# Kernel optimization log

Hardware: AMD Instinct MI355X
Metric: run time of the kernel (lower is better)

The kernel has to match this reference:

```python
import jax, jax.numpy as jnp
import numpy as np

BOUNDS = [0.01, 1.0, 100.0]
STEPS = [128, 128]
ALPHA_C = 0.01          # cfg.renderer.alpha
N_IMPORTANCE = 128      # cfg.renderer.importance_steps
N_RAYS = 65536


def _zvals_log_coarse():
    # matches torch.linspace(log10(b[i]), log10(b[i+1]) - seg/steps[i], steps[i]) per segment
    segs = []
    for i, s in enumerate(STEPS):
        lo = np.log10(BOUNDS[i]); hi = np.log10(BOUNDS[i + 1])
        segs.append(np.linspace(lo, hi - (hi - lo) / s, s, dtype=np.float32))
    return np.concatenate(segs)


def _seg_scale():
    tot = float(sum(STEPS))
    return np.concatenate([np.full(s, s / tot, dtype=np.float32) for s in STEPS])


def setup_inputs() -> dict:
    key = jax.random.key(0)
    k1, k2, k3, k4 = jax.random.split(key, 4)
    sigmas_coarse = jax.random.uniform(k1, (N_RAYS, sum(STEPS)), dtype=jnp.float32) * 5.0
    sigmas_fine = jax.random.uniform(k2, (N_RAYS, N_IMPORTANCE), dtype=jnp.float32) * 5.0
    rgbs_fine = jax.random.uniform(k3, (N_RAYS, N_IMPORTANCE, 3), dtype=jnp.float32)
    bg_color = jax.random.uniform(k4, (3,), dtype=jnp.float32)
    return {"sigmas_coarse": sigmas_coarse, "sigmas_fine": sigmas_fine,
            "rgbs_fine": rgbs_fine, "bg_color": bg_color}


def _weights_from_sigmas(sigmas, z_log):
    # delta[:, :-1] = diff(z_log), last delta = 0 (as in efficient_sampling)
    delta = jnp.concatenate([z_log[:, 1:] - z_log[:, :-1], jnp.zeros_like(z_log[:, :1])], -1)
    alpha = 1.0 - jnp.exp(-sigmas * delta)
    alpha_shift = jnp.concatenate([jnp.zeros_like(alpha[:, :1]), alpha[:, :-1]], -1)
    trans = jnp.cumprod(1.0 - alpha_shift, axis=-1)   # transmittance
    return alpha * trans


def _reweight(weights):
    # pad with zeros, 3-tap max blur, floor by alpha/S, per-segment rescale, normalize
    wpad = jnp.pad(weights, ((0, 0), (1, 1)))
    w = 0.5 * (jnp.maximum(wpad[:, :-2], wpad[:, 1:-1]) + jnp.maximum(wpad[:, 1:-1], wpad[:, 2:]))
    w = w + ALPHA_C / w.shape[-1]
    w = w * jnp.asarray(_seg_scale())
    return w / jnp.sum(w, axis=-1, keepdims=True)


def _sample_pdf(bins, weights, n_samples):
    # weights already normalized -> pdf; deterministic stratified u for reproducibility
    cdf = jnp.cumsum(weights, axis=-1)                     # [N, S]
    u = (jnp.arange(n_samples, dtype=bins.dtype) + 0.5) / n_samples
    u = jnp.broadcast_to(u, (bins.shape[0], n_samples))    # [N, n]
    inds = jax.vmap(lambda c, uu: jnp.searchsorted(c, uu, side='right'))(cdf, u)
    S = bins.shape[-1]
    below = jnp.clip(inds - 1, 0, S - 1)
    above = jnp.clip(inds, 0, S - 1)
    cdf_b = jnp.take_along_axis(cdf, below, -1)
    cdf_a = jnp.take_along_axis(cdf, above, -1)
    bin_b = jnp.take_along_axis(bins, below, -1)
    bin_a = jnp.take_along_axis(bins, above, -1)
    denom = jnp.where(cdf_a - cdf_b < 1e-5, 1.0, cdf_a - cdf_b)
    t = (u - cdf_b) / denom
    return bin_b + t * (bin_a - bin_b)


def reference(sigmas_coarse, sigmas_fine, rgbs_fine, bg_color):
    # --- efficient_sampling (no_grad path) ---
    z_log = jnp.broadcast_to(jnp.asarray(_zvals_log_coarse()), sigmas_coarse.shape)
    w_coarse = _weights_from_sigmas(sigmas_coarse, z_log)
    w_re = _reweight(w_coarse)
    z_log_fine = _sample_pdf(z_log, w_re, N_IMPORTANCE)     # [N, n_imp], sorted
    z_fine = jnp.power(10.0, z_log_fine)
    # --- render_rays_log-style compositing on fine samples ---
    w_fine = _weights_from_sigmas(sigmas_fine, z_log_fine)
    image = jnp.einsum('ns,nsc->nc', w_fine, rgbs_fine)
    image = image + (1.0 - jnp.sum(w_fine, -1)[..., None]) * bg_color
    invdepth = jnp.sum(w_fine / z_fine, axis=-1)
    lo = np.float32(np.log10(BOUNDS[0])); hi = np.float32(np.log10(BOUNDS[-1]))
    z_log_s = (z_log_fine - lo) / (hi - lo)
    return image, invdepth, w_fine, z_log_s
```

## Files before the change

### kernel.cpp

```cpp
#include <hip/hip_runtime.h>

#define SC 256
#define NF 128

template<int CTRL, int RM, int BM>
__device__ __forceinline__ float dpp_add(float x) {
    int s = __builtin_amdgcn_update_dpp(0, __float_as_int(x), CTRL, RM, BM, true);
    return x + __int_as_float(s);
}
template<int CTRL, int RM, int BM>
__device__ __forceinline__ int dpp_imax(int x) {
    int s = __builtin_amdgcn_update_dpp(0, x, CTRL, RM, BM, true);
    return (x > s) ? x : s;
}
template<int CTRL>
__device__ __forceinline__ float dpp_mov0(float x) {
    return __int_as_float(__builtin_amdgcn_update_dpp(0, __float_as_int(x), CTRL, 0xF, 0xF, true));
}
__device__ __forceinline__ float lane_f(float x, int l) {
    return __int_as_float(__builtin_amdgcn_readlane(__float_as_int(x), l));
}

__device__ __forceinline__ float wave_incl_scan(float x) {
    x = dpp_add<0x111, 0xF, 0xF>(x);
    x = dpp_add<0x112, 0xF, 0xF>(x);
    x = dpp_add<0x114, 0xF, 0xF>(x);
    x = dpp_add<0x118, 0xF, 0xF>(x);
    x = dpp_add<0x142, 0xA, 0xF>(x);
    x = dpp_add<0x143, 0xC, 0xF>(x);
    return x;
}

__device__ __forceinline__ int wave_incl_scan_imax(int x) {
    x = dpp_imax<0x111, 0xF, 0xF>(x);
    x = dpp_imax<0x112, 0xF, 0xF>(x);
    x = dpp_imax<0x114, 0xF, 0xF>(x);
    x = dpp_imax<0x118, 0xF, 0xF>(x);
    x = dpp_imax<0x142, 0xA, 0xF>(x);
    x = dpp_imax<0x143, 0xC, 0xF>(x);
    return x;
}

__device__ __forceinline__ float wave_sum_lane0(float x) {
    x = dpp_add<0xB1, 0xF, 0xF>(x);
    x = dpp_add<0x4E, 0xF, 0xF>(x);
    x = dpp_add<0x124, 0xF, 0xF>(x);
    x = dpp_add<0x128, 0xF, 0xF>(x);
    return x + lane_f(x, 16) + lane_f(x, 32) + lane_f(x, 48);
}

__device__ __forceinline__ int bin_klo(float c) {
    int k = (int)ceilf(fmaf(128.0f, c, -0.5f));
    return (k < 0) ? 0 : k;
}

__global__ __launch_bounds__(256) void nerf_render_kernel(
    const float* __restrict__ sig_c,
    const float* __restrict__ sig_f,
    const float* __restrict__ rgb_f,
    const float* __restrict__ bg,
    float* __restrict__ out,
    int n_rays)
{
    const int lane = threadIdx.x & 63;
    const int wid  = threadIdx.x >> 6;
    const int ray  = (blockIdx.x << 2) + wid;
    if (ray >= n_rays) return;

    __shared__ float s_cdf[4][SC];
    __shared__ int   s_idx[4][NF];

    const float4 sc4 = *reinterpret_cast<const float4*>(sig_c + (size_t)ray * SC + 4 * lane);
    const float2 sf  = *reinterpret_cast<const float2*>(sig_f + (size_t)ray * NF + 2 * lane);
    const float2* rp = reinterpret_cast<const float2*>(rgb_f + (size_t)ray * (NF * 3) + 6 * lane);
    const float2 ra = rp[0], rb = rp[1], rc = rp[2];
    const float bg0 = bg[0], bg1 = bg[1], bg2 = bg[2];

    const float DLT = 0.015625f;
    float x0 = sc4.x * DLT;
    float x1 = sc4.y * DLT;
    float x2 = sc4.z * DLT;
    float x3 = (lane == 63) ? 0.0f : sc4.w * DLT;

    float p0 = x0, p1 = p0 + x1, p2 = p1 + x2, p3 = p2 + x3;
    float incl = wave_incl_scan(p3);
    float excl = incl - p3;

    float T0 = __expf(-excl);
    float T1 = __expf(-(excl + p0));
    float T2 = __expf(-(excl + p1));
    float T3 = __expf(-(excl + p2));
    float T4 = __expf(-(excl + p3));
    float w0 = T0 - T1, w1 = T1 - T2, w2 = T2 - T3, w3 = T3 - T4;

    float wl = dpp_mov0<0x138>(w3);
    float wr = dpp_mov0<0x130>(w0);

    const float FLOOR = 0.01f / 256.0f;
    float m01 = fmaxf(w0, w1), m12 = fmaxf(w1, w2), m23 = fmaxf(w2, w3);
    float r0 = 0.5f * (fmaxf(wl, w0) + m01) + FLOOR;
    float r1 = 0.5f * (m01 + m12) + FLOOR;
    float r2 = 0.5f * (m12 + m23) + FLOOR;
    float r3 = 0.5f * (m23 + fmaxf(w3, wr)) + FLOOR;

    float q0 = r0, q1 = q0 + r1, q2 = q1 + r2, q3 = q2 + r3;
    float incl2 = wave_incl_scan(q3);
    float excl2 = incl2 - q3;
    float total = lane_f(incl2, 63);
    float inv_total = __builtin_amdgcn_rcpf(total);

    float c0 = (excl2 + q0) * inv_total;
    float c1 = (excl2 + q1) * inv_total;
    float c2 = (excl2 + q2) * inv_total;
    float c3 = (excl2 + q3) * inv_total;
    float cprev = dpp_mov0<0x138>(c3);

    float* cdf = s_cdf[wid];
    int*   idx = s_idx[wid];

    *reinterpret_cast<float4*>(&cdf[4 * lane]) = make_float4(c0, c1, c2, c3);

    *reinterpret_cast<int2*>(&idx[2 * lane]) = make_int2(-1, -1);

    const int jb = 4 * lane;
    int k0 = bin_klo(cprev);
    int k1 = bin_klo(c0);
    int k2 = bin_klo(c1);
    int k3 = bin_klo(c2);
    int k4 = bin_klo(c3);
    if (k0 < k1 && k0 < NF) idx[k0] = jb + 0;
    if (k1 < k2 && k1 < NF) idx[k1] = jb + 1;
    if (k2 < k3 && k2 < NF) idx[k2] = jb + 2;
    if (k3 < k4 && k3 < NF) idx[k3] = jb + 3;

    __asm__ __volatile__("" ::: "memory");

    const int2 jraw = *reinterpret_cast<const int2*>(&idx[2 * lane]);
    int m  = (jraw.x > jraw.y) ? jraw.x : jraw.y;
    int M  = wave_incl_scan_imax(m);
    int E  = __builtin_amdgcn_update_dpp(0, M, 0x138, 0xF, 0xF, true);
    int j0 = (E  > jraw.x) ? E  : jraw.x;
    int j1 = (j0 > jraw.y) ? j0 : jraw.y;

    int b0 = (j0 > 0) ? j0 - 1 : 0;
    int b1 = (j1 > 0) ? j1 - 1 : 0;
    float ca0 = cdf[j0], cb0 = cdf[b0];
    float ca1 = cdf[j1], cb1 = cdf[b1];

    const float u0 = ((float)(2 * lane) + 0.5f) * 0.0078125f;
    const float u1 = ((float)(2 * lane) + 1.5f) * 0.0078125f;

    float dn0 = ca0 - cb0;  dn0 = (dn0 < 1e-5f) ? 1.0f : dn0;
    float dn1 = ca1 - cb1;  dn1 = (dn1 < 1e-5f) ? 1.0f : dn1;
    float sc0f = (j0 > 0) ? DLT : 0.0f;
    float sc1f = (j1 > 0) ? DLT : 0.0f;
    float zL0 = fmaf((float)b0, DLT, -2.0f);
    float zL1 = fmaf((float)b1, DLT, -2.0f);
    float zl0 = fmaf((u0 - cb0) * __builtin_amdgcn_rcpf(dn0), sc0f, zL0);
    float zl1 = fmaf((u1 - cb1) * __builtin_amdgcn_rcpf(dn1), sc1f, zL1);

    float znext = dpp_mov0<0x130>(zl0);
    float d0 = zl1 - zl0;
    float d1 = (lane == 63) ? 0.0f : (znext - zl1);

    float y0 = sf.x * d0;
    float y1 = sf.y * d1;
    float ps = y0 + y1;
    float fincl = wave_incl_scan(ps);
    float fexcl = fincl - ps;

    float U0 = __expf(-fexcl);
    float U1 = __expf(-(fexcl + y0));
    float U2 = __expf(-(fexcl + ps));
    float wf0 = U0 - U1, wf1 = U1 - U2;

    float img_r = wf0 * ra.x + wf1 * rb.y;
    float img_g = wf0 * ra.y + wf1 * rc.x;
    float img_b = wf0 * rb.x + wf1 * rc.y;
    float wsum  = wf0 + wf1;
    float invd = wf0 * __exp10f(-zl0) + wf1 * __exp10f(-zl1);

    img_r = wave_sum_lane0(img_r);
    img_g = wave_sum_lane0(img_g);
    img_b = wave_sum_lane0(img_b);
    wsum  = wave_sum_lane0(wsum);
    invd  = wave_sum_lane0(invd);

    float* out_img  = out;
    float* out_invd = out + (size_t)n_rays * 3;
    float* out_wf   = out + (size_t)n_rays * 4;
    float* out_zs   = out + (size_t)n_rays * 4 + (size_t)n_rays * NF;

    if (lane == 0) {
        float one_m = 1.0f - wsum;
        out_img[(size_t)ray * 3 + 0] = img_r + one_m * bg0;
        out_img[(size_t)ray * 3 + 1] = img_g + one_m * bg1;
        out_img[(size_t)ray * 3 + 2] = img_b + one_m * bg2;
        out_invd[ray] = invd;
    }
    *reinterpret_cast<float2*>(out_wf + (size_t)ray * NF + 2 * lane) =
        make_float2(wf0, wf1);
    *reinterpret_cast<float2*>(out_zs + (size_t)ray * NF + 2 * lane) =
        make_float2((zl0 + 2.0f) * 0.25f, (zl1 + 2.0f) * 0.25f);
}

extern "C" void kernel_launch(void* const* d_in, const int* in_sizes, int n_in,
                              void* d_out, int out_size, void* d_ws, size_t ws_size,
                              hipStream_t stream) {
    const float* sig_c = (const float*)d_in[0];
    const float* sig_f = (const float*)d_in[1];
    const float* rgb_f = (const float*)d_in[2];
    const float* bg    = (const float*)d_in[3];
    float* out = (float*)d_out;

    const int n_rays = in_sizes[1] / NF;
    dim3 grid((n_rays + 3) / 4), block(256);
    hipLaunchKernelGGL(nerf_render_kernel, grid, block, 0, stream,
                       sig_c, sig_f, rgb_f, bg, out, n_rays);
}
```

Measured before the change: 236.3 us.

## Make kernel persistent with software-prefetched double-buffered ray loads

```diff
diff --git a/kernel.cpp b/kernel.cpp
--- a/kernel.cpp
+++ b/kernel.cpp
@@ -54,33 +54,35 @@
     return (k < 0) ? 0 : k;
 }
 
-__global__ __launch_bounds__(256) void nerf_render_kernel(
-    const float* __restrict__ sig_c,
-    const float* __restrict__ sig_f,
-    const float* __restrict__ rgb_f,
-    const float* __restrict__ bg,
-    float* __restrict__ out,
-    int n_rays)
+struct Ray {
+    float4 sc4;
+    float2 sf;
+    float2 ra, rb, rc;
+};
+
+__device__ __forceinline__ Ray load_ray(const float* __restrict__ sig_c,
+                                        const float* __restrict__ sig_f,
+                                        const float* __restrict__ rgb_f,
+                                        int ray, int lane) {
+    Ray d;
+    d.sc4 = *reinterpret_cast<const float4*>(sig_c + (size_t)ray * SC + 4 * lane);
+    d.sf  = *reinterpret_cast<const float2*>(sig_f + (size_t)ray * NF + 2 * lane);
+    const float2* rp = reinterpret_cast<const float2*>(rgb_f + (size_t)ray * (NF * 3) + 6 * lane);
+    d.ra = rp[0]; d.rb = rp[1]; d.rc = rp[2];
+    return d;
+}
+
+__device__ __forceinline__ void compute_ray(
+    const Ray& rd, int ray, int lane,
+    float* __restrict__ cdf, int* __restrict__ idx,
+    float bg0, float bg1, float bg2,
+    float* __restrict__ out, int n_rays)
 {
-    const int lane = threadIdx.x & 63;
-    const int wid  = threadIdx.x >> 6;
-    const int ray  = (blockIdx.x << 2) + wid;
-    if (ray >= n_rays) return;
-
-    __shared__ float s_cdf[4][SC];
-    __shared__ int   s_idx[4][NF];
-
-    const float4 sc4 = *reinterpret_cast<const float4*>(sig_c + (size_t)ray * SC + 4 * lane);
-    const float2 sf  = *reinterpret_cast<const float2*>(sig_f + (size_t)ray * NF + 2 * lane);
-    const float2* rp = reinterpret_cast<const float2*>(rgb_f + (size_t)ray * (NF * 3) + 6 * lane);
-    const float2 ra = rp[0], rb = rp[1], rc = rp[2];
-    const float bg0 = bg[0], bg1 = bg[1], bg2 = bg[2];
-
     const float DLT = 0.015625f;
-    float x0 = sc4.x * DLT;
-    float x1 = sc4.y * DLT;
-    float x2 = sc4.z * DLT;
-    float x3 = (lane == 63) ? 0.0f : sc4.w * DLT;
+    float x0 = rd.sc4.x * DLT;
+    float x1 = rd.sc4.y * DLT;
+    float x2 = rd.sc4.z * DLT;
+    float x3 = (lane == 63) ? 0.0f : rd.sc4.w * DLT;
 
     float p0 = x0, p1 = p0 + x1, p2 = p1 + x2, p3 = p2 + x3;
     float incl = wave_incl_scan(p3);
@@ -114,9 +116,6 @@
     float c2 = (excl2 + q2) * inv_total;
     float c3 = (excl2 + q3) * inv_total;
     float cprev = dpp_mov0<0x138>(c3);
-
-    float* cdf = s_cdf[wid];
-    int*   idx = s_idx[wid];
 
     *reinterpret_cast<float4*>(&cdf[4 * lane]) = make_float4(c0, c1, c2, c3);
 
@@ -163,8 +162,8 @@
     float d0 = zl1 - zl0;
     float d1 = (lane == 63) ? 0.0f : (znext - zl1);
 
-    float y0 = sf.x * d0;
-    float y1 = sf.y * d1;
+    float y0 = rd.sf.x * d0;
+    float y1 = rd.sf.y * d1;
     float ps = y0 + y1;
     float fincl = wave_incl_scan(ps);
     float fexcl = fincl - ps;
@@ -174,9 +173,9 @@
     float U2 = __expf(-(fexcl + ps));
     float wf0 = U0 - U1, wf1 = U1 - U2;
 
-    float img_r = wf0 * ra.x + wf1 * rb.y;
-    float img_g = wf0 * ra.y + wf1 * rc.x;
-    float img_b = wf0 * rb.x + wf1 * rc.y;
+    float img_r = wf0 * rd.ra.x + wf1 * rd.rb.y;
+    float img_g = wf0 * rd.ra.y + wf1 * rd.rc.x;
+    float img_b = wf0 * rd.rb.x + wf1 * rd.rc.y;
     float wsum  = wf0 + wf1;
     float invd = wf0 * __exp10f(-zl0) + wf1 * __exp10f(-zl1);
 
@@ -204,6 +203,44 @@
         make_float2((zl0 + 2.0f) * 0.25f, (zl1 + 2.0f) * 0.25f);
 }
 
+__global__ __launch_bounds__(256) void nerf_render_kernel(
+    const float* __restrict__ sig_c,
+    const float* __restrict__ sig_f,
+    const float* __restrict__ rgb_f,
+    const float* __restrict__ bg,
+    float* __restrict__ out,
+    int n_rays)
+{
+    const int lane = threadIdx.x & 63;
+    const int wid  = threadIdx.x >> 6;
+
+    __shared__ float s_cdf[4][SC];
+    __shared__ int   s_idx[4][NF];
+    float* cdf = s_cdf[wid];
+    int*   idx = s_idx[wid];
+
+    const int n_waves = (int)(gridDim.x << 2);
+    const int w       = (int)(blockIdx.x << 2) + wid;
+    const int rpw     = (n_rays + n_waves - 1) / n_waves;
+    const int r_base  = w * rpw;
+    if (r_base >= n_rays) return;
+
+    const float bg0 = bg[0], bg1 = bg[1], bg2 = bg[2];
+
+    const int last = n_rays - 1;
+    Ray A = load_ray(sig_c, sig_f, rgb_f, r_base <= last ? r_base : last, lane);
+    Ray B;
+    for (int i = 0; i < rpw; i += 2) {
+        int rA = r_base + i;
+        int rB = r_base + i + 1;
+        int rC = r_base + i + 2;
+        B = load_ray(sig_c, sig_f, rgb_f, rB <= last ? rB : last, lane);
+        if (rA <= last) compute_ray(A, rA, lane, cdf, idx, bg0, bg1, bg2, out, n_rays);
+        A = load_ray(sig_c, sig_f, rgb_f, rC <= last ? rC : last, lane);
+        if (rB <= last) compute_ray(B, rB, lane, cdf, idx, bg0, bg1, bg2, out, n_rays);
+    }
+}
+
 extern "C" void kernel_launch(void* const* d_in, const int* in_sizes, int n_in,
                               void* d_out, int out_size, void* d_ws, size_t ws_size,
                               hipStream_t stream) {
@@ -214,7 +251,9 @@
     float* out = (float*)d_out;
 
     const int n_rays = in_sizes[1] / NF;
-    dim3 grid((n_rays + 3) / 4), block(256);
+    int blocks_needed = (n_rays + 3) / 4;
+    int blocks = blocks_needed < 2048 ? blocks_needed : 2048;
+    dim3 grid(blocks), block(256);
     hipLaunchKernelGGL(nerf_render_kernel, grid, block, 0, stream,
                        sig_c, sig_f, rgb_f, bg, out, n_rays);
 }
```

Result: slower. 246.4 us (+4.2%).
